# Performance work log

Hardware: AMD Instinct MI355X
Metric: run time of the kernel (lower is better)

## Reference

```python
import jax, jax.numpy as jnp
import numpy as np

DIM = 512
HEADS = 8
DIM_HEAD = 64
HIDDEN = HEADS * DIM_HEAD  # 512
B, C, H, W = 32, DIM, 32, 32


def setup_inputs() -> dict:
    key = jax.random.key(0)
    ks = jax.random.split(key, 7)
    s_in = 1.0 / np.sqrt(DIM)
    s_h = 1.0 / np.sqrt(HIDDEN)
    x = jax.random.normal(ks[0], (B, C, H, W), dtype=jnp.float32)
    Wq = jax.random.uniform(ks[1], (DIM, HIDDEN), jnp.float32, -s_in, s_in)
    Wk = jax.random.uniform(ks[2], (DIM, HIDDEN), jnp.float32, -s_in, s_in)
    Wv = jax.random.uniform(ks[3], (DIM, HIDDEN), jnp.float32, -s_in, s_in)
    Wp = jax.random.uniform(ks[4], (HIDDEN, DIM), jnp.float32, -s_h, s_h)
    bp = jax.random.uniform(ks[5], (DIM,), jnp.float32, -s_h, s_h)
    return {"x": x, "Wq": Wq, "Wk": Wk, "Wv": Wv, "Wp": Wp, "bp": bp}


def reference(x, Wq, Wk, Wv, Wp, bp):
    b, c, h, w = x.shape
    n = h * w
    xt = x.reshape(b, c, n).transpose(0, 2, 1)  # [B, N, C]
    q = (xt @ Wq).reshape(b, n, HEADS, DIM_HEAD)
    k = (xt @ Wk).reshape(b, n, HEADS, DIM_HEAD)
    v = (xt @ Wv).reshape(b, n, HEADS, DIM_HEAD)
    k_softmax = jax.nn.softmax(k, axis=1)  # softmax over tokens N
    context = jnp.einsum('bnhd,bnhv->bhdv', k_softmax, v)  # [B, H, D, D]
    out = jnp.einsum('bnhd,bhdv->bnhv', q, context).reshape(b, n, HIDDEN)
    out = out @ Wp + bp  # [B, N, C]
    return out.transpose(0, 2, 1).reshape(b, c, h, w)
```

## Files before the change

kernel.cpp:

```cpp
#include <hip/hip_runtime.h>
#include <hip/hip_bf16.h>


__device__ __forceinline__ float bf2f(unsigned short u) {
    union { unsigned int i; float f; } x;
    x.i = ((unsigned int)u) << 16;
    return x.f;
}
__device__ __forceinline__ unsigned short f2bf(float f) {
    unsigned int u = __float_as_uint(f);
    unsigned int lsb = (u >> 16) & 1u;
    u += 0x7fffu + lsb;
    return (unsigned short)(u >> 16);
}

__device__ __forceinline__ void glds16(const unsigned short* g, unsigned short* l) {
    __builtin_amdgcn_global_load_lds(
        (const __attribute__((address_space(1))) unsigned int*)g,
        (__attribute__((address_space(3))) unsigned int*)l,
        16, 0, 0);
}

typedef __bf16 bf16x8 __attribute__((ext_vector_type(8)));
typedef float  f32x4  __attribute__((ext_vector_type(4)));

__global__ __launch_bounds__(256) void transpose_x(
    const void* __restrict__ in, unsigned short* __restrict__ out,
    int* __restrict__ flag)
{
    const int t = threadIdx.x;
    const unsigned short* xs = (const unsigned short*)in;
    unsigned short u0 = xs[2 * (t & 63)];
    int e0 = (u0 >> 7) & 0xFF;
    unsigned long long bm = __ballot(e0 >= 113 && e0 <= 142);
    const int fl = (__popcll(bm) >= 32) ? 1 : 0;
    if (blockIdx.x == 0 && blockIdx.y == 0 && blockIdx.z == 0 && t == 0)
        *flag = fl;

    const int b  = blockIdx.z;
    const int c0 = blockIdx.x * 64;
    const int r0 = blockIdx.y * 64;
    __shared__ unsigned short Ts[64][68];
    const int tr  = t >> 4;
    const int tc4 = (t & 15) * 4;
    #pragma unroll
    for (int rr = 0; rr < 4; ++rr) {
        int rl = rr * 16 + tr;
        long off = (long)b * 524288 + (long)(r0 + rl) * 1024 + c0 + tc4;
        unsigned short v[4];
        if (fl) {
            ushort4 u = *(const ushort4*)((const unsigned short*)in + off);
            v[0] = u.x; v[1] = u.y; v[2] = u.z; v[3] = u.w;
        } else {
            float4 u = *(const float4*)((const float*)in + off);
            v[0] = f2bf(u.x); v[1] = f2bf(u.y); v[2] = f2bf(u.z); v[3] = f2bf(u.w);
        }
        #pragma unroll
        for (int q = 0; q < 4; ++q) Ts[tc4 + q][rl] = v[q];
    }
    __syncthreads();
    #pragma unroll
    for (int rr = 0; rr < 4; ++rr) {
        int cl = rr * 16 + tr;
        ushort4 o = *(const ushort4*)&Ts[cl][tc4];
        *(ushort4*)(out + (long)b * 524288 + (long)(c0 + cl) * 512 + r0 + tc4) = o;
    }
}

__global__ __launch_bounds__(256) void transpose_w3(
    const void* __restrict__ w0, const void* __restrict__ w1,
    const void* __restrict__ w2, unsigned short* __restrict__ out,
    unsigned short* __restrict__ wqb,
    const int* __restrict__ flag)
{
    const int fl = *flag;
    const int z  = blockIdx.z;
    const void* in = (z == 0) ? w0 : (z == 1) ? w1 : w2;
    unsigned short* op = out + (long)z * 262144;
    const int c0 = blockIdx.x * 64;
    const int r0 = blockIdx.y * 64;
    __shared__ unsigned short Ts[64][68];
    const int t   = threadIdx.x;
    const int tr  = t >> 4;
    const int tc4 = (t & 15) * 4;
    #pragma unroll
    for (int rr = 0; rr < 4; ++rr) {
        int rl = rr * 16 + tr;
        long off = (long)(r0 + rl) * 512 + c0 + tc4;
        unsigned short v[4];
        if (fl) {
            ushort4 u = *(const ushort4*)((const unsigned short*)in + off);
            v[0] = u.x; v[1] = u.y; v[2] = u.z; v[3] = u.w;
        } else {
            float4 u = *(const float4*)((const float*)in + off);
            v[0] = f2bf(u.x); v[1] = f2bf(u.y); v[2] = f2bf(u.z); v[3] = f2bf(u.w);
        }
        if (z == 0) {
            ushort4 s; s.x = v[0]; s.y = v[1]; s.z = v[2]; s.w = v[3];
            *(ushort4*)(wqb + off) = s;
        }
        #pragma unroll
        for (int q = 0; q < 4; ++q) Ts[tc4 + q][rl] = v[q];
    }
    __syncthreads();
    #pragma unroll
    for (int rr = 0; rr < 4; ++rr) {
        int cl = rr * 16 + tr;
        ushort4 o = *(const ushort4*)&Ts[cl][tc4];
        *(ushort4*)(op + (long)(c0 + cl) * 512 + r0 + tc4) = o;
    }
}

__global__ __launch_bounds__(1024, 4) void gemm_bt_256(
    const unsigned short* __restrict__ A, long a_bstride,
    const unsigned short* __restrict__ Bm, long b_bstride,
    void* __restrict__ C, long c_bstride,
    const void* __restrict__ bias,
    int M, int N, int K, int mode,
    const int* __restrict__ flag)
{
    const int gx = gridDim.x, gy = gridDim.y;
    const int nwg = gx * gy * (int)gridDim.z;
    const int lid = blockIdx.x + gx * (blockIdx.y + gy * blockIdx.z);
    const int swzid = (lid & 7) * (nwg >> 3) + (lid >> 3);
    const int bx = swzid % gx;
    const int by = (swzid / gx) % gy;
    const int bz = swzid / (gx * gy);

    const int b  = bz;
    const int n0 = bx * 256;
    const int m0 = by * 256;
    const unsigned short* Ab = A  + (long)b * a_bstride;
    const unsigned short* Bb = Bm + (long)b * b_bstride;

    __shared__ unsigned short S[65536];

    const int t  = threadIdx.x;
    const int w  = t >> 6;
    const int l  = t & 63;
    const int fm = l & 15;
    const int kg = l >> 4;
    const int wr = w >> 2;
    const int wc = w & 3;

    const int rowb = w * 8 + (l >> 3);
    const int swz  = ((l & 7) ^ (l >> 3)) * 8;
    const unsigned short* gA = Ab + (long)(m0 + rowb) * K + swz;
    const unsigned short* gB = Bb + (long)(n0 + rowb) * K + swz;

    const int sA = fm & 7;

    f32x4 acc[4][4] = {};

    const int NT = K >> 6;

    auto STAGE = [&](int kt, int buf) {
        const long ko = (long)kt * 64;
        unsigned short* Ld = &S[buf * 32768];
        #pragma unroll
        for (int r = 0; r < 2; ++r)
            glds16(gA + (long)r * 128 * K + ko, Ld + (r * 128 + w * 8) * 64);
        #pragma unroll
        for (int r = 0; r < 2; ++r)
            glds16(gB + (long)r * 128 * K + ko, Ld + 16384 + (r * 128 + w * 8) * 64);
    };

    STAGE(0, 0);

    for (int tt = 0; tt < NT; ++tt) {
        if (tt + 1 < NT) {
            STAGE(tt + 1, (tt + 1) & 1);
            __builtin_amdgcn_sched_barrier(0);
            asm volatile("s_waitcnt vmcnt(4)" ::: "memory");
        } else {
            __builtin_amdgcn_sched_barrier(0);
            asm volatile("s_waitcnt vmcnt(0)" ::: "memory");
        }
        __builtin_amdgcn_sched_barrier(0);
        __builtin_amdgcn_s_barrier();
        __builtin_amdgcn_sched_barrier(0);

        {
            const unsigned short* Abuf = &S[(tt & 1) * 32768];
            const unsigned short* Bbuf = Abuf + 16384;
            bf16x8 bf[4][2];
            #pragma unroll
            for (int j = 0; j < 4; ++j)
                #pragma unroll
                for (int kk = 0; kk < 2; ++kk) {
                    const int row = wc * 64 + j * 16 + fm;
                    bf[j][kk] = *(const bf16x8*)&Bbuf[row * 64 + ((kk * 4 + kg) ^ sA) * 8];
                }
            #pragma unroll
            for (int i = 0; i < 4; ++i) {
                bf16x8 af[2];
                #pragma unroll
                for (int kk = 0; kk < 2; ++kk) {
                    const int row = wr * 64 + i * 16 + fm;
                    af[kk] = *(const bf16x8*)&Abuf[row * 64 + ((kk * 4 + kg) ^ sA) * 8];
                }
                __builtin_amdgcn_s_setprio(1);
                #pragma unroll
                for (int j = 0; j < 4; ++j)
                    #pragma unroll
                    for (int kk = 0; kk < 2; ++kk)
                        acc[i][j] = __builtin_amdgcn_mfma_f32_16x16x32_bf16(
                            bf[j][kk], af[kk], acc[i][j], 0, 0, 0);
                __builtin_amdgcn_s_setprio(0);
            }
        }

        __builtin_amdgcn_sched_barrier(0);
        __builtin_amdgcn_s_barrier();
        __builtin_amdgcn_sched_barrier(0);
    }

    const int fl = *flag;
    const long cb = (long)b * c_bstride;
    #pragma unroll
    for (int i = 0; i < 4; ++i) {
        const int m = m0 + wr * 64 + i * 16 + fm;
        float bv = 0.f;
        if (mode == 2 && bias)
            bv = fl ? bf2f(((const unsigned short*)bias)[m])
                    : ((const float*)bias)[m];
        #pragma unroll
        for (int j = 0; j < 4; ++j) {
            const int nb = n0 + wc * 64 + j * 16 + kg * 4;
            const long off = cb + (long)m * N + nb;
            if (mode == 0) {
                ushort4 o;
                o.x = f2bf(acc[i][j][0]); o.y = f2bf(acc[i][j][1]);
                o.z = f2bf(acc[i][j][2]); o.w = f2bf(acc[i][j][3]);
                *(ushort4*)&((unsigned short*)C)[off] = o;
            } else if (fl) {
                ushort4 o;
                o.x = f2bf(acc[i][j][0] + bv); o.y = f2bf(acc[i][j][1] + bv);
                o.z = f2bf(acc[i][j][2] + bv); o.w = f2bf(acc[i][j][3] + bv);
                *(ushort4*)&((unsigned short*)C)[off] = o;
            } else {
                float4 o;
                o.x = acc[i][j][0] + bv; o.y = acc[i][j][1] + bv;
                o.z = acc[i][j][2] + bv; o.w = acc[i][j][3] + bv;
                *(float4*)&((float*)C)[off] = o;
            }
        }
    }
}

__global__ __launch_bounds__(256) void gemm_bt_mfma(
    const unsigned short* __restrict__ A, long a_bstride,
    const unsigned short* __restrict__ Bm, long b_bstride,
    void* __restrict__ C, long c_bstride,
    const void* __restrict__ bias,
    int M, int N, int K, int mode,
    const int* __restrict__ flag)
{
    const int b  = blockIdx.z;
    const int n0 = blockIdx.x * 128;
    const int m0 = blockIdx.y * 128;
    const unsigned short* Ab = A  + (long)b * a_bstride;
    const unsigned short* Bb = Bm + (long)b * b_bstride;

    __shared__ unsigned short As[2 * 128 * 32];
    __shared__ unsigned short Bs[2 * 128 * 32];

    const int t    = threadIdx.x;
    const int w    = t >> 6;
    const int lane = t & 63;
    const int wm   = (w & 1) * 64;
    const int wn   = (w >> 1) * 64;
    const int fm   = lane & 15;
    const int kg   = lane >> 4;

    const int crow = lane >> 2;
    const int ccol = (lane & 3) * 8;

    f32x4 acc[4][4] = {};

    #pragma unroll
    for (int j = 0; j < 2; ++j) {
        const int chunk = w * 2 + j;
        const int row   = chunk * 16 + crow;
        glds16(Ab + (long)(m0 + row) * K + ccol, &As[chunk * 512]);
        glds16(Bb + (long)(n0 + row) * K + ccol, &Bs[chunk * 512]);
    }

    int cur = 0;
    for (int k0 = 0; k0 < K; k0 += 32) {
        __syncthreads();

        if (k0 + 32 < K) {
            const int kn  = k0 + 32;
            const int nxt = (cur ^ 1) * 4096;
            #pragma unroll
            for (int j = 0; j < 2; ++j) {
                const int chunk = w * 2 + j;
                const int row   = chunk * 16 + crow;
                glds16(Ab + (long)(m0 + row) * K + kn + ccol, &As[nxt + chunk * 512]);
                glds16(Bb + (long)(n0 + row) * K + kn + ccol, &Bs[nxt + chunk * 512]);
            }
        }

        const int bufo = cur * 4096;
        bf16x8 af[4], bf[4];
        #pragma unroll
        for (int i = 0; i < 4; ++i)
            af[i] = *(const bf16x8*)&As[bufo + (wm + i * 16 + fm) * 32 + kg * 8];
        #pragma unroll
        for (int j = 0; j < 4; ++j)
            bf[j] = *(const bf16x8*)&Bs[bufo + (wn + j * 16 + fm) * 32 + kg * 8];
        #pragma unroll
        for (int i = 0; i < 4; ++i)
            #pragma unroll
            for (int j = 0; j < 4; ++j)
                acc[i][j] = __builtin_amdgcn_mfma_f32_16x16x32_bf16(
                    bf[j], af[i], acc[i][j], 0, 0, 0);
        cur ^= 1;
    }

    const int fl = *flag;
    const long cb = (long)b * c_bstride;
    #pragma unroll
    for (int i = 0; i < 4; ++i) {
        const int m = m0 + wm + i * 16 + fm;
        float bv = 0.f;
        if (mode == 2 && bias)
            bv = fl ? bf2f(((const unsigned short*)bias)[m])
                    : ((const float*)bias)[m];
        #pragma unroll
        for (int j = 0; j < 4; ++j) {
            const int nb = n0 + wn + j * 16 + kg * 4;
            const long off = cb + (long)m * N + nb;
            if (mode == 0) {
                ushort4 o;
                o.x = f2bf(acc[i][j][0]); o.y = f2bf(acc[i][j][1]);
                o.z = f2bf(acc[i][j][2]); o.w = f2bf(acc[i][j][3]);
                *(ushort4*)&((unsigned short*)C)[off] = o;
            } else if (fl) {
                ushort4 o;
                o.x = f2bf(acc[i][j][0] + bv); o.y = f2bf(acc[i][j][1] + bv);
                o.z = f2bf(acc[i][j][2] + bv); o.w = f2bf(acc[i][j][3] + bv);
                *(ushort4*)&((unsigned short*)C)[off] = o;
            } else {
                float4 o;
                o.x = acc[i][j][0] + bv; o.y = acc[i][j][1] + bv;
                o.z = acc[i][j][2] + bv; o.w = acc[i][j][3] + bv;
                *(float4*)&((float*)C)[off] = o;
            }
        }
    }
}

__global__ __launch_bounds__(256) void ctx_softmax_mfma(
    const unsigned short* __restrict__ KV, float* __restrict__ ctx)
{
    const int bh = blockIdx.x;
    const unsigned short* Kb = KV + ((long)(bh >> 3) << 20) + (long)(bh & 7) * 65536;
    const unsigned short* Vb = Kb + 524288;

    const int t    = threadIdx.x;
    const int w    = t >> 6;
    const int lane = t & 63;
    const int fm   = lane & 15;
    const int kg   = lane >> 4;

    f32x4 acc[4][4] = {};
    float sloc[4] = {0.f, 0.f, 0.f, 0.f};

    #pragma unroll 2
    for (int c = 0; c < 8; ++c) {
        const int k0 = w * 256 + c * 32;
        bf16x8 af[4], bf[4];
        #pragma unroll
        for (int i = 0; i < 4; ++i) {
            uint4 u = *(const uint4*)(Kb + (long)(i * 16 + fm) * 1024 + k0 + kg * 8);
            unsigned short o[8];
            #pragma unroll
            for (int z = 0; z < 4; ++z) {
                unsigned int uu = ((const unsigned int*)&u)[z];
                float lo = __expf(bf2f((unsigned short)(uu & 0xffffu)));
                float hi = __expf(bf2f((unsigned short)(uu >> 16)));
                sloc[i] += lo + hi;
                o[2 * z]     = f2bf(lo);
                o[2 * z + 1] = f2bf(hi);
            }
            af[i] = *(const bf16x8*)o;
        }
        #pragma unroll
        for (int j = 0; j < 4; ++j)
            bf[j] = *(const bf16x8*)(Vb + (long)(j * 16 + fm) * 1024 + k0 + kg * 8);
        #pragma unroll
        for (int i = 0; i < 4; ++i)
            #pragma unroll
            for (int j = 0; j < 4; ++j)
                acc[i][j] = __builtin_amdgcn_mfma_f32_16x16x32_bf16(
                    af[i], bf[j], acc[i][j], 0, 0, 0);
    }

    __shared__ float sred[4][64];
    __shared__ float sinv[64];
    #pragma unroll
    for (int i = 0; i < 4; ++i) {
        sloc[i] += __shfl_xor(sloc[i], 16, 64);
        sloc[i] += __shfl_xor(sloc[i], 32, 64);
    }
    if (kg == 0) {
        #pragma unroll
        for (int i = 0; i < 4; ++i) sred[w][i * 16 + fm] = sloc[i];
    }
    __syncthreads();
    if (t < 64) sinv[t] = 1.0f / (sred[0][t] + sred[1][t] + sred[2][t] + sred[3][t]);

    __shared__ float red[64][65];
    for (int ph = 0; ph < 4; ++ph) {
        __syncthreads();
        if (w == ph) {
            #pragma unroll
            for (int i = 0; i < 4; ++i)
                #pragma unroll
                for (int j = 0; j < 4; ++j)
                    #pragma unroll
                    for (int r = 0; r < 4; ++r) {
                        const int m = i * 16 + kg * 4 + r;
                        const int n = j * 16 + fm;
                        if (ph == 0) red[m][n]  = acc[i][j][r];
                        else         red[m][n] += acc[i][j][r];
                    }
        }
    }
    __syncthreads();
    float* cp = ctx + (long)bh * 4096;
    for (int i = t; i < 4096; i += 256)
        cp[i] = red[i >> 6][i & 63] * sinv[i >> 6];
}

__global__ __launch_bounds__(256) void weff_kernel(
    const float* __restrict__ ctx,
    const void* __restrict__ Wp,
    unsigned short* __restrict__ WeffT,
    const int* __restrict__ flag)
{
    const int fl = *flag;
    const int c0 = blockIdx.x * 64;
    const int h  = blockIdx.y;
    const int b  = blockIdx.z;

    __shared__ float Cs[64][65];
    __shared__ float Ws[64][68];

    const int t = threadIdx.x;
    const int tx = t & 15, ty = t >> 4;

    const float* cb = ctx + ((long)b * 8 + h) * 4096;
    for (int i = t; i < 4096; i += 256) Cs[i >> 6][i & 63] = cb[i];
    for (int i = t; i < 4096; i += 256) {
        int v = i >> 6, c = i & 63;
        long idx = (long)(h * 64 + v) * 512 + c0 + c;
        Ws[v][c] = fl ? bf2f(((const unsigned short*)Wp)[idx])
                      : ((const float*)Wp)[idx];
    }
    __syncthreads();

    float acc[4][4];
    #pragma unroll
    for (int i = 0; i < 4; ++i)
        #pragma unroll
        for (int j = 0; j < 4; ++j) acc[i][j] = 0.f;

    #pragma unroll
    for (int v = 0; v < 64; ++v) {
        float a[4], d[4];
        #pragma unroll
        for (int i = 0; i < 4; ++i) a[i] = Ws[v][ty * 4 + i];
        #pragma unroll
        for (int j = 0; j < 4; ++j) d[j] = Cs[tx * 4 + j][v];
        #pragma unroll
        for (int i = 0; i < 4; ++i)
            #pragma unroll
            for (int j = 0; j < 4; ++j) acc[i][j] += a[i] * d[j];
    }
    #pragma unroll
    for (int i = 0; i < 4; ++i) {
        ushort4 o;
        o.x = f2bf(acc[i][0]); o.y = f2bf(acc[i][1]);
        o.z = f2bf(acc[i][2]); o.w = f2bf(acc[i][3]);
        *(ushort4*)&WeffT[((long)b * 512 + c0 + ty * 4 + i) * 512 + h * 64 + tx * 4] = o;
    }
}

extern "C" void kernel_launch(void* const* d_in, const int* in_sizes, int n_in,
                              void* d_out, int out_size, void* d_ws, size_t ws_size,
                              hipStream_t stream) {
    const void* x  = d_in[0];
    const void* Wq = d_in[1];
    const void* Wk = d_in[2];
    const void* Wv = d_in[3];
    const void* Wp = d_in[4];
    const void* bp = d_in[5];

    char* ws = (char*)d_ws;
    unsigned short* Xt    = (unsigned short*)(ws);
    unsigned short* KV    = (unsigned short*)(ws + 33554432ll);
    unsigned short* Ft    = (unsigned short*)(ws + 33554432ll);
    float*          ctx   = (float*)(ws + 100663296ll);
    unsigned short* WeffT = (unsigned short*)(ws + 104857600ll);
    unsigned short* WT    = (unsigned short*)(ws + 121634816ll);
    unsigned short* Wqb   = (unsigned short*)(ws + 123207680ll);
    int*            flag  = (int*)(ws + 123731968ll);

    transpose_x<<<dim3(16, 8, 32), 256, 0, stream>>>(x, Xt, flag);
    transpose_w3<<<dim3(8, 8, 3), 256, 0, stream>>>(Wq, Wk, Wv, WT, Wqb, flag);

    const long XB = 1024ll * 512;
    gemm_bt_256<<<dim3(4, 4, 32), 1024, 0, stream>>>(
        WT + 262144, 0, Xt, XB, KV, 1048576ll, nullptr, 1024, 1024, 512, 0, flag);

    ctx_softmax_mfma<<<dim3(256), 256, 0, stream>>>(KV, ctx);

    weff_kernel<<<dim3(8, 8, 32), 256, 0, stream>>>(ctx, Wp, WeffT, flag);

    gemm_bt_mfma<<<dim3(4, 4, 32), 256, 0, stream>>>(
        WeffT, 262144ll, Wqb, 0, Ft, 262144ll, nullptr, 512, 512, 512, 0, flag);

    gemm_bt_256<<<dim3(4, 2, 32), 1024, 0, stream>>>(
        Ft, 262144ll, Xt, XB, d_out, 524288ll, bp, 512, 1024, 512, 2, flag);
}
```

Measured before the change: 284.1 us.

## Fuse softmax-context and Weff kernels into one 512-thread block per head

Merges the context computation (softmax over tokens plus K^T V via MFMA) with the Weff = ctx·Wp kernel, keeping the normalized context in shared memory instead of writing it to global and re-reading it. Blocks grow to 512 threads, with 8 waves splitting the token range. The cross-wave reduction becomes two passes into four LDS buffers plus a sum. Each block then loops over four column chunks of Wp with two half-blocks. This removes a launch and the fp32 ctx round trip, but leaves only 256 blocks for the Weff work and uses much more LDS per block.

```diff
diff --git a/kernel.cpp b/kernel.cpp
--- a/kernel.cpp
+++ b/kernel.cpp
@@ -352,11 +352,16 @@
     }
 }
 
-__global__ __launch_bounds__(256) void ctx_softmax_mfma(
-    const unsigned short* __restrict__ KV, float* __restrict__ ctx)
+__global__ __launch_bounds__(512) void ctx_weff_fused(
+    const unsigned short* __restrict__ KV,
+    const void* __restrict__ Wp,
+    unsigned short* __restrict__ WeffT,
+    const int* __restrict__ flag)
 {
     const int bh = blockIdx.x;
-    const unsigned short* Kb = KV + ((long)(bh >> 3) << 20) + (long)(bh & 7) * 65536;
+    const int b  = bh >> 3;
+    const int h  = bh & 7;
+    const unsigned short* Kb = KV + ((long)b << 20) + (long)h * 65536;
     const unsigned short* Vb = Kb + 524288;
 
     const int t    = threadIdx.x;
@@ -365,12 +370,17 @@
     const int fm   = lane & 15;
     const int kg   = lane >> 4;
 
+    __shared__ float red4[4][64][65];
+    __shared__ float Ws[2][64][68];
+    __shared__ float sred[8][64];
+    __shared__ float sinv[64];
+
     f32x4 acc[4][4] = {};
     float sloc[4] = {0.f, 0.f, 0.f, 0.f};
 
-    #pragma unroll 2
-    for (int c = 0; c < 8; ++c) {
-        const int k0 = w * 256 + c * 32;
+    #pragma unroll
+    for (int c = 0; c < 4; ++c) {
+        const int k0 = w * 128 + c * 32;
         bf16x8 af[4], bf[4];
         #pragma unroll
         for (int i = 0; i < 4; ++i) {
@@ -398,8 +408,6 @@
                     af[i], bf[j], acc[i][j], 0, 0, 0);
     }
 
-    __shared__ float sred[4][64];
-    __shared__ float sinv[64];
     #pragma unroll
     for (int i = 0; i < 4; ++i) {
         sloc[i] += __shfl_xor(sloc[i], 16, 64);
@@ -409,83 +417,81 @@
         #pragma unroll
         for (int i = 0; i < 4; ++i) sred[w][i * 16 + fm] = sloc[i];
     }
+
+    if (w < 4) {
+        #pragma unroll
+        for (int i = 0; i < 4; ++i)
+            #pragma unroll
+            for (int j = 0; j < 4; ++j)
+                #pragma unroll
+                for (int r = 0; r < 4; ++r)
+                    red4[w][i * 16 + kg * 4 + r][j * 16 + fm] = acc[i][j][r];
+    }
     __syncthreads();
-    if (t < 64) sinv[t] = 1.0f / (sred[0][t] + sred[1][t] + sred[2][t] + sred[3][t]);
-
-    __shared__ float red[64][65];
-    for (int ph = 0; ph < 4; ++ph) {
+    if (w >= 4) {
+        #pragma unroll
+        for (int i = 0; i < 4; ++i)
+            #pragma unroll
+            for (int j = 0; j < 4; ++j)
+                #pragma unroll
+                for (int r = 0; r < 4; ++r)
+                    red4[w - 4][i * 16 + kg * 4 + r][j * 16 + fm] += acc[i][j][r];
+    }
+    if (t < 64) {
+        float s = 0.f;
+        #pragma unroll
+        for (int q = 0; q < 8; ++q) s += sred[q][t];
+        sinv[t] = 1.0f / s;
+    }
+    __syncthreads();
+    for (int i = t; i < 4096; i += 512) {
+        const int m = i >> 6, n = i & 63;
+        red4[0][m][n] = (red4[0][m][n] + red4[1][m][n] +
+                         red4[2][m][n] + red4[3][m][n]) * sinv[m];
+    }
+    __syncthreads();
+
+    const int fl   = *flag;
+    const int half = t >> 8;
+    const int th   = t & 255;
+    const int tx   = th & 15, ty = th >> 4;
+
+    for (int chunk = 0; chunk < 4; ++chunk) {
+        const int c0 = chunk * 128 + half * 64;
+        for (int i = th; i < 4096; i += 256) {
+            const int v = i >> 6, c = i & 63;
+            const long idx = (long)(h * 64 + v) * 512 + c0 + c;
+            Ws[half][v][c] = fl ? bf2f(((const unsigned short*)Wp)[idx])
+                                : ((const float*)Wp)[idx];
+        }
         __syncthreads();
-        if (w == ph) {
+
+        float wacc[4][4];
+        #pragma unroll
+        for (int i = 0; i < 4; ++i)
+            #pragma unroll
+            for (int j = 0; j < 4; ++j) wacc[i][j] = 0.f;
+
+        #pragma unroll 8
+        for (int v = 0; v < 64; ++v) {
+            float a[4], d[4];
+            #pragma unroll
+            for (int i = 0; i < 4; ++i) a[i] = Ws[half][v][ty * 4 + i];
+            #pragma unroll
+            for (int j = 0; j < 4; ++j) d[j] = red4[0][tx * 4 + j][v];
             #pragma unroll
             for (int i = 0; i < 4; ++i)
                 #pragma unroll
-                for (int j = 0; j < 4; ++j)
-                    #pragma unroll
-                    for (int r = 0; r < 4; ++r) {
-                        const int m = i * 16 + kg * 4 + r;
-                        const int n = j * 16 + fm;
-                        if (ph == 0) red[m][n]  = acc[i][j][r];
-                        else         red[m][n] += acc[i][j][r];
-                    }
-        }
-    }
-    __syncthreads();
-    float* cp = ctx + (long)bh * 4096;
-    for (int i = t; i < 4096; i += 256)
-        cp[i] = red[i >> 6][i & 63] * sinv[i >> 6];
-}
-
-__global__ __launch_bounds__(256) void weff_kernel(
-    const float* __restrict__ ctx,
-    const void* __restrict__ Wp,
-    unsigned short* __restrict__ WeffT,
-    const int* __restrict__ flag)
-{
-    const int fl = *flag;
-    const int c0 = blockIdx.x * 64;
-    const int h  = blockIdx.y;
-    const int b  = blockIdx.z;
-
-    __shared__ float Cs[64][65];
-    __shared__ float Ws[64][68];
-
-    const int t = threadIdx.x;
-    const int tx = t & 15, ty = t >> 4;
-
-    const float* cb = ctx + ((long)b * 8 + h) * 4096;
-    for (int i = t; i < 4096; i += 256) Cs[i >> 6][i & 63] = cb[i];
-    for (int i = t; i < 4096; i += 256) {
-        int v = i >> 6, c = i & 63;
-        long idx = (long)(h * 64 + v) * 512 + c0 + c;
-        Ws[v][c] = fl ? bf2f(((const unsigned short*)Wp)[idx])
-                      : ((const float*)Wp)[idx];
-    }
-    __syncthreads();
-
-    float acc[4][4];
-    #pragma unroll
-    for (int i = 0; i < 4; ++i)
-        #pragma unroll
-        for (int j = 0; j < 4; ++j) acc[i][j] = 0.f;
-
-    #pragma unroll
-    for (int v = 0; v < 64; ++v) {
-        float a[4], d[4];
-        #pragma unroll
-        for (int i = 0; i < 4; ++i) a[i] = Ws[v][ty * 4 + i];
-        #pragma unroll
-        for (int j = 0; j < 4; ++j) d[j] = Cs[tx * 4 + j][v];
-        #pragma unroll
-        for (int i = 0; i < 4; ++i)
-            #pragma unroll
-            for (int j = 0; j < 4; ++j) acc[i][j] += a[i] * d[j];
-    }
-    #pragma unroll
-    for (int i = 0; i < 4; ++i) {
-        ushort4 o;
-        o.x = f2bf(acc[i][0]); o.y = f2bf(acc[i][1]);
-        o.z = f2bf(acc[i][2]); o.w = f2bf(acc[i][3]);
-        *(ushort4*)&WeffT[((long)b * 512 + c0 + ty * 4 + i) * 512 + h * 64 + tx * 4] = o;
+                for (int j = 0; j < 4; ++j) wacc[i][j] += a[i] * d[j];
+        }
+        #pragma unroll
+        for (int i = 0; i < 4; ++i) {
+            ushort4 o;
+            o.x = f2bf(wacc[i][0]); o.y = f2bf(wacc[i][1]);
+            o.z = f2bf(wacc[i][2]); o.w = f2bf(wacc[i][3]);
+            *(ushort4*)&WeffT[((long)b * 512 + c0 + ty * 4 + i) * 512 + h * 64 + tx * 4] = o;
+        }
+        __syncthreads();
     }
 }
 
@@ -503,7 +509,6 @@
     unsigned short* Xt    = (unsigned short*)(ws);
     unsigned short* KV    = (unsigned short*)(ws + 33554432ll);
     unsigned short* Ft    = (unsigned short*)(ws + 33554432ll);
-    float*          ctx   = (float*)(ws + 100663296ll);
     unsigned short* WeffT = (unsigned short*)(ws + 104857600ll);
     unsigned short* WT    = (unsigned short*)(ws + 121634816ll);
     unsigned short* Wqb   = (unsigned short*)(ws + 123207680ll);
@@ -516,9 +521,7 @@
     gemm_bt_256<<<dim3(4, 4, 32), 1024, 0, stream>>>(
         WT + 262144, 0, Xt, XB, KV, 1048576ll, nullptr, 1024, 1024, 512, 0, flag);
 
-    ctx_softmax_mfma<<<dim3(256), 256, 0, stream>>>(KV, ctx);
-
-    weff_kernel<<<dim3(8, 8, 32), 256, 0, stream>>>(ctx, Wp, WeffT, flag);
+    ctx_weff_fused<<<dim3(256), 512, 0, stream>>>(KV, Wp, WeffT, flag);
 
     gemm_bt_mfma<<<dim3(4, 4, 32), 256, 0, stream>>>(
         WeffT, 262144ll, Wqb, 0, Ft, 262144ll, nullptr, 512, 512, 512, 0, flag);
```

Result: slower. 291.9 us (+2.8%).
